# Kernel optimization log

Measured on AMD Instinct MI355X. Metric: run time of the kernel, lower is better.

Reference implementation:

```python
import jax, jax.numpy as jnp
import numpy as np
import math

B, T, C = 8, 1024, 1024
E, K = 8, 2
H = 4 * C


def new_gelu(x):
    # tanh-approx GELU, identical to the torch reference
    c = math.sqrt(2.0 / math.pi)
    return 0.5 * x * (1.0 + jnp.tanh(c * (x + 0.044715 * x ** 3)))


def setup_inputs() -> dict:
    key = jax.random.key(0)
    ks = jax.random.split(key, 4)
    x = jax.random.normal(ks[0], (B, T, C), dtype=jnp.float32)
    # router: nn.Linear(C, E, bias=False), weight [E, C], init std=0.02
    router_w = 0.02 * jax.random.normal(ks[1], (E, C), dtype=jnp.float32)
    # stacked expert MLP weights (bias=False): c_fc [E, C, H], c_proj [E, H, C]
    w_fc = 0.02 * jax.random.normal(ks[2], (E, C, H), dtype=jnp.float32)
    w_proj = 0.02 * jax.random.normal(ks[3], (E, H, C), dtype=jnp.float32)
    return {"x": x, "router_w": router_w, "w_fc": w_fc, "w_proj": w_proj}


def reference(x, router_w, w_fc, w_proj):
    n_expert = w_fc.shape[0]
    seq_rep = x.mean(axis=1)                                  # [B, C]
    router_logits = seq_rep @ router_w.T                      # [B, E]
    probs_full = jax.nn.softmax(router_logits.astype(jnp.float32), axis=-1)
    probs = probs_full.astype(x.dtype)
    weights, sel = jax.lax.top_k(probs, K)                    # [B, K]
    weights = weights / weights.sum(axis=-1, keepdims=True)

    # gather selected expert weights and run grouped dense MLPs
    w1 = w_fc[sel]                                            # [B, K, C, H]
    w2 = w_proj[sel]                                          # [B, K, H, C]
    h = new_gelu(jnp.einsum('btc,bkch->bkth', x, w1))         # [B, K, T, H]
    out_k = jnp.einsum('bkth,bkhc->bktc', h, w2)              # [B, K, T, C]
    final_output = jnp.einsum('bk,bktc->btc', weights, out_k)

    # load balancing loss
    Bf = jnp.asarray(x.shape[0], jnp.float32)
    expert_importance = probs_full.sum(axis=0) / Bf           # [E]
    is_assigned = jnp.zeros_like(probs_full).at[jnp.arange(x.shape[0])[:, None], sel].set(1.0)
    expert_load = is_assigned.sum(axis=0) / Bf                # [E]
    load_balancing_loss = n_expert * jnp.sum(expert_importance * expert_load)
    return final_output, load_balancing_loss
```

## Files before the change

### kernel.cpp

```cpp
#include <hip/hip_runtime.h>

#define B_ 8
#define T_ 1024
#define C_ 1024
#define E_ 8
#define H_ 4096

typedef float v4f __attribute__((ext_vector_type(4)));
typedef short v8s __attribute__((ext_vector_type(8)));

__device__ __forceinline__ unsigned short f2bf(float f) {
  union { float f; unsigned int u; } x; x.f = f;
  unsigned int r = x.u + 0x7fffu + ((x.u >> 16) & 1u);
  return (unsigned short)(r >> 16);
}

__device__ __forceinline__ void async_load16(const unsigned short* g, unsigned short* l) {
  __builtin_amdgcn_global_load_lds(
      (const __attribute__((address_space(1))) void*)g,
      (__attribute__((address_space(3))) void*)l, 16, 0, 0);
}


__global__ void k_meanpart(const float* __restrict__ x, float* __restrict__ part) {
  int b = blockIdx.x >> 3, tc = blockIdx.x & 7;
  int c4 = threadIdx.x * 4;
  const float* xp = x + (size_t)b * T_ * C_ + (size_t)tc * 128 * C_ + c4;
  v4f s = {0.f, 0.f, 0.f, 0.f};
  for (int t = 0; t < 128; ++t) s += *(const v4f*)(xp + (size_t)t * C_);
  *(v4f*)(part + (size_t)(tc * B_ + b) * C_ + c4) = s;
}

__global__ void k_router(const float* __restrict__ part, const float* __restrict__ rw,
                         int* __restrict__ sel, float* __restrict__ wv,
                         float* __restrict__ loss_out) {
  __shared__ float seq[B_ * C_];
  __shared__ float pr[B_][E_];
  __shared__ int ss[B_][2];
  const int tid = threadIdx.x;
  for (int idx = tid; idx < B_ * C_; idx += 256) {
    float s = 0.f;
#pragma unroll
    for (int tc = 0; tc < 8; ++tc) s += part[(size_t)tc * B_ * C_ + idx];
    seq[idx] = s * (1.0f / T_);
  }
  __syncthreads();
  if (tid < B_ * E_) {
    int b = tid >> 3, e = tid & 7;
    float acc = 0.f;
    for (int c = 0; c < C_; ++c) acc += seq[b * C_ + c] * rw[e * C_ + c];
    pr[b][e] = acc;
  }
  __syncthreads();
  if (tid < B_) {
    int b = tid;
    float mx = pr[b][0];
#pragma unroll
    for (int e = 1; e < E_; ++e) mx = fmaxf(mx, pr[b][e]);
    float p[E_]; float sum = 0.f;
#pragma unroll
    for (int e = 0; e < E_; ++e) { p[e] = __expf(pr[b][e] - mx); sum += p[e]; }
    float inv = 1.0f / sum;
#pragma unroll
    for (int e = 0; e < E_; ++e) { p[e] *= inv; pr[b][e] = p[e]; }
    int i0 = 0;
#pragma unroll
    for (int e = 1; e < E_; ++e) if (p[e] > p[i0]) i0 = e;
    int i1 = (i0 == 0) ? 1 : 0;
#pragma unroll
    for (int e = 0; e < E_; ++e) if (e != i0 && p[e] > p[i1]) i1 = e;
    float s2 = p[i0] + p[i1];
    sel[b * 2 + 0] = i0; sel[b * 2 + 1] = i1;
    wv[b * 2 + 0] = p[i0] / s2; wv[b * 2 + 1] = p[i1] / s2;
    ss[b][0] = i0; ss[b][1] = i1;
  }
  __syncthreads();
  if (tid == 0) {
    float loss = 0.f;
    for (int e = 0; e < E_; ++e) {
      float imp = 0.f, ld = 0.f;
      for (int b = 0; b < B_; ++b) {
        imp += pr[b][e];
        ld += ((ss[b][0] == e) || (ss[b][1] == e)) ? 1.f : 0.f;
      }
      loss += (imp / (float)B_) * (ld / (float)B_);
    }
    loss_out[0] = loss * (float)E_;
  }
}


__global__ void k_castx(const float* __restrict__ x, unsigned short* __restrict__ xb) {
  size_t i = (size_t)blockIdx.x * 256 + threadIdx.x;
  v4f v = *(const v4f*)(x + i * 4);
  ushort4 o;
  o.x = f2bf(v.x); o.y = f2bf(v.y); o.z = f2bf(v.z); o.w = f2bf(v.w);
  *(ushort4*)(xb + i * 4) = o;
}

__global__ void k_transpose(const float* __restrict__ src, unsigned short* __restrict__ dst,
                            int R, int Cc) {
  __shared__ float tile[32][33];
  const size_t sl = (size_t)blockIdx.z * R * Cc;
  int c0 = blockIdx.x * 32, r0 = blockIdx.y * 32;
  int tx = threadIdx.x & 31, ty = threadIdx.x >> 5;
#pragma unroll
  for (int j = ty; j < 32; j += 8)
    tile[j][tx] = src[sl + (size_t)(r0 + j) * Cc + c0 + tx];
  __syncthreads();
#pragma unroll
  for (int j = ty; j < 32; j += 8)
    dst[sl + (size_t)(c0 + j) * R + r0 + tx] = f2bf(tile[tx][j]);
}


__device__ __forceinline__ void gemm_seg(const unsigned short* A, int lda,
                                         const unsigned short* Bt, int ldb,
                                         int Kd, int row0, int col0,
                                         unsigned short* As, unsigned short* Bs,
                                         v4f (&acc)[4][4]) {
  const int tid = threadIdx.x;
  const int lane = tid & 63;
  const int wave = __builtin_amdgcn_readfirstlane(tid >> 6);
  const int r = lane & 15, q = lane >> 4;
  const int wm = wave & 1, wn = wave >> 1;
  const int lrow = lane >> 2, lch = lane & 3;
  const bool doA = (wave < 2);
  const int jb = (wave & 1) * 4;
  const int gld = doA ? lda : ldb;
  const unsigned short* gbase =
      (doA ? (A + (size_t)row0 * lda) : (Bt + (size_t)col0 * ldb)) +
      (size_t)(jb * 16 + lrow) * gld + lch * 8;
  unsigned short* lbase = (doA ? As : Bs) + jb * 512;

  for (int kc = 0; kc < Kd; kc += 32) {
    const unsigned short* g = gbase + kc;
    async_load16(g + 0 * 16 * (size_t)gld, lbase + 0 * 512);
    async_load16(g + 1 * 16 * (size_t)gld, lbase + 1 * 512);
    async_load16(g + 2 * 16 * (size_t)gld, lbase + 2 * 512);
    async_load16(g + 3 * 16 * (size_t)gld, lbase + 3 * 512);
    __syncthreads();
    v8s af[4], bf[4];
#pragma unroll
    for (int i = 0; i < 4; ++i)
      af[i] = *(const v8s*)&As[(wm * 64 + i * 16 + r) * 32 + q * 8];
#pragma unroll
    for (int j = 0; j < 4; ++j)
      bf[j] = *(const v8s*)&Bs[(wn * 64 + j * 16 + r) * 32 + q * 8];
#pragma unroll
    for (int i = 0; i < 4; ++i)
#pragma unroll
      for (int j = 0; j < 4; ++j)
        acc[i][j] = __builtin_amdgcn_mfma_f32_16x16x32_bf16(af[i], bf[j], acc[i][j], 0, 0, 0);
    __syncthreads();
  }
}

__global__ __launch_bounds__(256, 2) void k_gemm1(
    const unsigned short* __restrict__ Xb, const unsigned short* __restrict__ Wfct,
    const int* __restrict__ sel, const float* __restrict__ wv,
    unsigned short* __restrict__ Hout) {
  __shared__ unsigned short As[128 * 32];
  __shared__ unsigned short Bs[128 * 32];
  const int bk = blockIdx.z;
  const int e = sel[bk];
  const float wgt = wv[bk];
  const int row0 = blockIdx.y * 128, col0 = blockIdx.x * 128;
  v4f acc[4][4];
#pragma unroll
  for (int i = 0; i < 4; ++i)
#pragma unroll
    for (int j = 0; j < 4; ++j) acc[i][j] = (v4f){0.f, 0.f, 0.f, 0.f};

  gemm_seg(Xb + (size_t)(bk >> 1) * T_ * C_, C_, Wfct + (size_t)e * H_ * C_, C_,
           C_, row0, col0, As, Bs, acc);

  const int lane = threadIdx.x & 63;
  const int wave = threadIdx.x >> 6;
  const int r = lane & 15, q = lane >> 4;
  const int wm = wave & 1, wn = wave >> 1;
  unsigned short* Co = Hout + (size_t)bk * T_ * H_;
#pragma unroll
  for (int i = 0; i < 4; ++i) {
    int gr = row0 + wm * 64 + i * 16 + q * 4;
#pragma unroll
    for (int j = 0; j < 4; ++j) {
      int gc = col0 + wn * 64 + j * 16 + r;
#pragma unroll
      for (int p = 0; p < 4; ++p) {
        float u = acc[i][j][p];
        float y = 0.7978845608028654f * (u + 0.044715f * u * u * u);
        float t = 1.0f - 2.0f / (__expf(2.0f * y) + 1.0f);
        float gv = 0.5f * u * (1.0f + t) * wgt;
        Co[(size_t)(gr + p) * H_ + gc] = f2bf(gv);
      }
    }
  }
}

__global__ __launch_bounds__(256, 2) void k_gemm2(
    const unsigned short* __restrict__ Hin, const unsigned short* __restrict__ Wpt,
    const int* __restrict__ sel, float* __restrict__ Out) {
  __shared__ unsigned short As[128 * 32];
  __shared__ unsigned short Bs[128 * 32];
  const int b = blockIdx.z;
  const int row0 = blockIdx.y * 128, col0 = blockIdx.x * 128;
  v4f acc[4][4];
#pragma unroll
  for (int i = 0; i < 4; ++i)
#pragma unroll
    for (int j = 0; j < 4; ++j) acc[i][j] = (v4f){0.f, 0.f, 0.f, 0.f};

  for (int k = 0; k < 2; ++k) {
    int e = sel[b * 2 + k];
    gemm_seg(Hin + (size_t)(b * 2 + k) * T_ * H_, H_, Wpt + (size_t)e * C_ * H_, H_,
             H_, row0, col0, As, Bs, acc);
  }

  const int lane = threadIdx.x & 63;
  const int wave = threadIdx.x >> 6;
  const int r = lane & 15, q = lane >> 4;
  const int wm = wave & 1, wn = wave >> 1;
  float* Co = Out + (size_t)b * T_ * C_;
#pragma unroll
  for (int i = 0; i < 4; ++i) {
    int gr = row0 + wm * 64 + i * 16 + q * 4;
#pragma unroll
    for (int j = 0; j < 4; ++j) {
      int gc = col0 + wn * 64 + j * 16 + r;
#pragma unroll
      for (int p = 0; p < 4; ++p)
        Co[(size_t)(gr + p) * C_ + gc] = acc[i][j][p];
    }
  }
}


extern "C" void kernel_launch(void* const* d_in, const int* in_sizes, int n_in,
                              void* d_out, int out_size, void* d_ws, size_t ws_size,
                              hipStream_t stream) {
  const float* x   = (const float*)d_in[0];
  const float* rw  = (const float*)d_in[1];
  const float* wfc = (const float*)d_in[2];
  const float* wpj = (const float*)d_in[3];
  float* out = (float*)d_out;
  char* ws = (char*)d_ws;

  float*          part = (float*)(ws + 0);
  int*            sel  = (int*)(ws + (262144));
  float*          wv   = (float*)(ws + (262144 + 64));
  unsigned short* xb   = (unsigned short*)(ws + 524288);
  unsigned short* wfct = (unsigned short*)(ws + 524288 + 16777216);
  unsigned short* wpjt = (unsigned short*)(ws + 524288 + 16777216 + 67108864);
  unsigned short* h    = (unsigned short*)(ws + 524288 + 16777216 + 2*67108864ll);

  k_meanpart<<<dim3(B_ * 8), dim3(256), 0, stream>>>(x, part);
  k_router<<<dim3(1), dim3(256), 0, stream>>>(part, rw, sel, wv,
                                              out + (size_t)B_ * T_ * C_);
  k_castx<<<dim3((B_ * T_ * C_ / 4) / 256), dim3(256), 0, stream>>>(x, xb);
  k_transpose<<<dim3(H_ / 32, C_ / 32, E_), dim3(256), 0, stream>>>(wfc, wfct, C_, H_);
  k_transpose<<<dim3(C_ / 32, H_ / 32, E_), dim3(256), 0, stream>>>(wpj, wpjt, H_, C_);

  k_gemm1<<<dim3(H_ / 128, T_ / 128, B_ * 2), dim3(256), 0, stream>>>(xb, wfct, sel, wv, h);
  k_gemm2<<<dim3(C_ / 128, T_ / 128, B_), dim3(256), 0, stream>>>(h, wpjt, sel, out);
}
```

Measured before the change: 795.1 us.

## Fuse x cast into mean, widen transpose, coalesce GELU stores, split gemm2 by expert

The bf16 cast of x now happens inside the mean-reduction kernel, so x is read once and a separate cast launch goes away. The weight transpose uses 64x64 tiles with float4 loads and ushort4 stores for wider memory access. The gemm1 GELU epilogue is staged through LDS so H is written with coalesced 16-byte row stores, and both GEMMs request 4 blocks per CU. gemm2 now runs one block per (batch, expert) pair, writing into two partial buffers that a new add kernel sums. This doubles the parallelism of the second GEMM at the cost of extra fp32 traffic and one more launch.

```diff
diff --git a/kernel.cpp b/kernel.cpp
--- a/kernel.cpp
+++ b/kernel.cpp
@@ -22,12 +22,20 @@
 }
 
 
-__global__ void k_meanpart(const float* __restrict__ x, float* __restrict__ part) {
+__global__ void k_meanpart(const float* __restrict__ x, float* __restrict__ part,
+                           unsigned short* __restrict__ xb) {
   int b = blockIdx.x >> 3, tc = blockIdx.x & 7;
   int c4 = threadIdx.x * 4;
-  const float* xp = x + (size_t)b * T_ * C_ + (size_t)tc * 128 * C_ + c4;
+  const size_t base = (size_t)b * T_ * C_ + (size_t)tc * 128 * C_ + c4;
+  const float* xp = x + base;
   v4f s = {0.f, 0.f, 0.f, 0.f};
-  for (int t = 0; t < 128; ++t) s += *(const v4f*)(xp + (size_t)t * C_);
+  for (int t = 0; t < 128; ++t) {
+    v4f v = *(const v4f*)(xp + (size_t)t * C_);
+    s += v;
+    ushort4 o;
+    o.x = f2bf(v.x); o.y = f2bf(v.y); o.z = f2bf(v.z); o.w = f2bf(v.w);
+    *(ushort4*)(xb + base + (size_t)t * C_) = o;
+  }
   *(v4f*)(part + (size_t)(tc * B_ + b) * C_ + c4) = s;
 }
 
@@ -89,28 +97,29 @@
   }
 }
 
-
-__global__ void k_castx(const float* __restrict__ x, unsigned short* __restrict__ xb) {
-  size_t i = (size_t)blockIdx.x * 256 + threadIdx.x;
-  v4f v = *(const v4f*)(x + i * 4);
-  ushort4 o;
-  o.x = f2bf(v.x); o.y = f2bf(v.y); o.z = f2bf(v.z); o.w = f2bf(v.w);
-  *(ushort4*)(xb + i * 4) = o;
-}
-
 __global__ void k_transpose(const float* __restrict__ src, unsigned short* __restrict__ dst,
                             int R, int Cc) {
-  __shared__ float tile[32][33];
+  __shared__ float tile[64][65];
   const size_t sl = (size_t)blockIdx.z * R * Cc;
-  int c0 = blockIdx.x * 32, r0 = blockIdx.y * 32;
-  int tx = threadIdx.x & 31, ty = threadIdx.x >> 5;
-#pragma unroll
-  for (int j = ty; j < 32; j += 8)
-    tile[j][tx] = src[sl + (size_t)(r0 + j) * Cc + c0 + tx];
-  __syncthreads();
-#pragma unroll
-  for (int j = ty; j < 32; j += 8)
-    dst[sl + (size_t)(c0 + j) * R + r0 + tx] = f2bf(tile[tx][j]);
+  int c0 = blockIdx.x * 64, r0 = blockIdx.y * 64;
+  int tx = threadIdx.x & 15, ty = threadIdx.x >> 4;
+#pragma unroll
+  for (int p = 0; p < 4; ++p) {
+    int r = p * 16 + ty;
+    v4f v = *(const v4f*)(src + sl + (size_t)(r0 + r) * Cc + c0 + tx * 4);
+    tile[r][tx * 4 + 0] = v.x; tile[r][tx * 4 + 1] = v.y;
+    tile[r][tx * 4 + 2] = v.z; tile[r][tx * 4 + 3] = v.w;
+  }
+  __syncthreads();
+#pragma unroll
+  for (int p = 0; p < 4; ++p) {
+    int c = p * 16 + ty;
+    int rr = tx * 4;
+    ushort4 o;
+    o.x = f2bf(tile[rr + 0][c]); o.y = f2bf(tile[rr + 1][c]);
+    o.z = f2bf(tile[rr + 2][c]); o.w = f2bf(tile[rr + 3][c]);
+    *(ushort4*)(dst + sl + (size_t)(c0 + c) * R + r0 + rr) = o;
+  }
 }
 
 
@@ -156,12 +165,13 @@
   }
 }
 
-__global__ __launch_bounds__(256, 2) void k_gemm1(
+__global__ __launch_bounds__(256, 4) void k_gemm1(
     const unsigned short* __restrict__ Xb, const unsigned short* __restrict__ Wfct,
     const int* __restrict__ sel, const float* __restrict__ wv,
     unsigned short* __restrict__ Hout) {
-  __shared__ unsigned short As[128 * 32];
-  __shared__ unsigned short Bs[128 * 32];
+  __shared__ unsigned short SH[128 * 64];
+  unsigned short* As = SH;
+  unsigned short* Bs = SH + 128 * 32;
   const int bk = blockIdx.z;
   const int e = sel[bk];
   const float wgt = wv[bk];
@@ -175,11 +185,65 @@
   gemm_seg(Xb + (size_t)(bk >> 1) * T_ * C_, C_, Wfct + (size_t)e * H_ * C_, C_,
            C_, row0, col0, As, Bs, acc);
 
+  const int tid = threadIdx.x;
+  const int lane = tid & 63;
+  const int wave = tid >> 6;
+  const int r = lane & 15, q = lane >> 4;
+  const int wm = wave & 1, wn = wave >> 1;
+  unsigned short* Co = Hout + (size_t)bk * T_ * H_;
+#pragma unroll
+  for (int hh = 0; hh < 2; ++hh) {
+    if (wm == hh) {
+#pragma unroll
+      for (int i = 0; i < 4; ++i)
+#pragma unroll
+        for (int j = 0; j < 4; ++j)
+#pragma unroll
+          for (int p = 0; p < 4; ++p) {
+            int lr = i * 16 + q * 4 + p;
+            int lc = wn * 64 + j * 16 + r;
+            float u = acc[i][j][p];
+            float y = 0.7978845608028654f * (u + 0.044715f * u * u * u);
+            float t = 1.0f - 2.0f / (__expf(2.0f * y) + 1.0f);
+            SH[lr * 128 + lc] = f2bf(0.5f * u * (1.0f + t) * wgt);
+          }
+    }
+    __syncthreads();
+#pragma unroll
+    for (int it = 0; it < 4; ++it) {
+      int idx = it * 256 + tid;
+      int row = idx >> 4, ch = idx & 15;
+      *(v8s*)&Co[(size_t)(row0 + hh * 64 + row) * H_ + col0 + ch * 8] =
+          *(const v8s*)&SH[row * 128 + ch * 8];
+    }
+    __syncthreads();
+  }
+}
+
+__global__ __launch_bounds__(256, 4) void k_gemm2(
+    const unsigned short* __restrict__ Hin, const unsigned short* __restrict__ Wpt,
+    const int* __restrict__ sel, float* __restrict__ P0, float* __restrict__ P1) {
+  __shared__ unsigned short SH[128 * 64];
+  unsigned short* As = SH;
+  unsigned short* Bs = SH + 128 * 32;
+  const int bk = blockIdx.z;
+  const int b = bk >> 1, k = bk & 1;
+  const int e = sel[bk];
+  const int row0 = blockIdx.y * 128, col0 = blockIdx.x * 128;
+  v4f acc[4][4];
+#pragma unroll
+  for (int i = 0; i < 4; ++i)
+#pragma unroll
+    for (int j = 0; j < 4; ++j) acc[i][j] = (v4f){0.f, 0.f, 0.f, 0.f};
+
+  gemm_seg(Hin + (size_t)bk * T_ * H_, H_, Wpt + (size_t)e * C_ * H_, H_,
+           H_, row0, col0, As, Bs, acc);
+
   const int lane = threadIdx.x & 63;
   const int wave = threadIdx.x >> 6;
   const int r = lane & 15, q = lane >> 4;
   const int wm = wave & 1, wn = wave >> 1;
-  unsigned short* Co = Hout + (size_t)bk * T_ * H_;
+  float* Co = (k == 0 ? P0 : P1) + (size_t)b * T_ * C_;
 #pragma unroll
   for (int i = 0; i < 4; ++i) {
     int gr = row0 + wm * 64 + i * 16 + q * 4;
@@ -187,52 +251,18 @@
     for (int j = 0; j < 4; ++j) {
       int gc = col0 + wn * 64 + j * 16 + r;
 #pragma unroll
-      for (int p = 0; p < 4; ++p) {
-        float u = acc[i][j][p];
-        float y = 0.7978845608028654f * (u + 0.044715f * u * u * u);
-        float t = 1.0f - 2.0f / (__expf(2.0f * y) + 1.0f);
-        float gv = 0.5f * u * (1.0f + t) * wgt;
-        Co[(size_t)(gr + p) * H_ + gc] = f2bf(gv);
-      }
-    }
-  }
-}
-
-__global__ __launch_bounds__(256, 2) void k_gemm2(
-    const unsigned short* __restrict__ Hin, const unsigned short* __restrict__ Wpt,
-    const int* __restrict__ sel, float* __restrict__ Out) {
-  __shared__ unsigned short As[128 * 32];
-  __shared__ unsigned short Bs[128 * 32];
-  const int b = blockIdx.z;
-  const int row0 = blockIdx.y * 128, col0 = blockIdx.x * 128;
-  v4f acc[4][4];
-#pragma unroll
-  for (int i = 0; i < 4; ++i)
-#pragma unroll
-    for (int j = 0; j < 4; ++j) acc[i][j] = (v4f){0.f, 0.f, 0.f, 0.f};
-
-  for (int k = 0; k < 2; ++k) {
-    int e = sel[b * 2 + k];
-    gemm_seg(Hin + (size_t)(b * 2 + k) * T_ * H_, H_, Wpt + (size_t)e * C_ * H_, H_,
-             H_, row0, col0, As, Bs, acc);
-  }
-
-  const int lane = threadIdx.x & 63;
-  const int wave = threadIdx.x >> 6;
-  const int r = lane & 15, q = lane >> 4;
-  const int wm = wave & 1, wn = wave >> 1;
-  float* Co = Out + (size_t)b * T_ * C_;
-#pragma unroll
-  for (int i = 0; i < 4; ++i) {
-    int gr = row0 + wm * 64 + i * 16 + q * 4;
-#pragma unroll
-    for (int j = 0; j < 4; ++j) {
-      int gc = col0 + wn * 64 + j * 16 + r;
-#pragma unroll
       for (int p = 0; p < 4; ++p)
         Co[(size_t)(gr + p) * C_ + gc] = acc[i][j][p];
     }
   }
+}
+
+__global__ void k_add(float* __restrict__ out, const float* __restrict__ p1) {
+  size_t i = ((size_t)blockIdx.x * 256 + threadIdx.x) * 4;
+  v4f a = *(const v4f*)(out + i);
+  v4f b = *(const v4f*)(p1 + i);
+  a += b;
+  *(v4f*)(out + i) = a;
 }
 
 
@@ -247,20 +277,21 @@
   char* ws = (char*)d_ws;
 
   float*          part = (float*)(ws + 0);
-  int*            sel  = (int*)(ws + (262144));
-  float*          wv   = (float*)(ws + (262144 + 64));
+  int*            sel  = (int*)(ws + 262144);
+  float*          wv   = (float*)(ws + 262144 + 64);
   unsigned short* xb   = (unsigned short*)(ws + 524288);
   unsigned short* wfct = (unsigned short*)(ws + 524288 + 16777216);
   unsigned short* wpjt = (unsigned short*)(ws + 524288 + 16777216 + 67108864);
   unsigned short* h    = (unsigned short*)(ws + 524288 + 16777216 + 2*67108864ll);
-
-  k_meanpart<<<dim3(B_ * 8), dim3(256), 0, stream>>>(x, part);
+  float*          p1   = (float*)(ws + 524288);
+
+  k_meanpart<<<dim3(B_ * 8), dim3(256), 0, stream>>>(x, part, xb);
   k_router<<<dim3(1), dim3(256), 0, stream>>>(part, rw, sel, wv,
                                               out + (size_t)B_ * T_ * C_);
-  k_castx<<<dim3((B_ * T_ * C_ / 4) / 256), dim3(256), 0, stream>>>(x, xb);
-  k_transpose<<<dim3(H_ / 32, C_ / 32, E_), dim3(256), 0, stream>>>(wfc, wfct, C_, H_);
-  k_transpose<<<dim3(C_ / 32, H_ / 32, E_), dim3(256), 0, stream>>>(wpj, wpjt, H_, C_);
+  k_transpose<<<dim3(H_ / 64, C_ / 64, E_), dim3(256), 0, stream>>>(wfc, wfct, C_, H_);
+  k_transpose<<<dim3(C_ / 64, H_ / 64, E_), dim3(256), 0, stream>>>(wpj, wpjt, H_, C_);
 
   k_gemm1<<<dim3(H_ / 128, T_ / 128, B_ * 2), dim3(256), 0, stream>>>(xb, wfct, sel, wv, h);
-  k_gemm2<<<dim3(C_ / 128, T_ / 128, B_), dim3(256), 0, stream>>>(h, wpjt, sel, out);
-}
+  k_gemm2<<<dim3(C_ / 128, T_ / 128, B_ * 2), dim3(256), 0, stream>>>(h, wpjt, sel, out, p1);
+  k_add<<<dim3(B_ * T_ * C_ / 4 / 256), dim3(256), 0, stream>>>(out, p1);
+}
```

Result: no change. 795.9 us (+0.1%).
